# Kernel optimization log

Hardware: AMD Instinct MI355X
Metric: run time of the kernel (lower is better)

The kernel has to match this reference:

```python
import jax, jax.numpy as jnp
from jax import lax
import numpy as np

B, T, I, H, O = 64, 1024, 256, 512, 128


def setup_inputs() -> dict:
    key = jax.random.key(0)
    ks = jax.random.split(key, 12)
    s_i = 1.0 / np.sqrt(H)
    return {
        "x": jax.random.normal(ks[0], (B, T, I), dtype=jnp.float32),
        "h0": jnp.zeros((2, B, H), dtype=jnp.float32),
        # layer 0 RNNCell(I -> H)
        "W_ih0": jax.random.uniform(ks[1], (H, I), jnp.float32, -s_i, s_i),
        "b_ih0": jax.random.uniform(ks[2], (H,), jnp.float32, -s_i, s_i),
        "W_hh0": jax.random.uniform(ks[3], (H, H), jnp.float32, -s_i, s_i),
        "b_hh0": jax.random.uniform(ks[4], (H,), jnp.float32, -s_i, s_i),
        # layer 1 RNNCell(H -> H)
        "W_ih1": jax.random.uniform(ks[5], (H, H), jnp.float32, -s_i, s_i),
        "b_ih1": jax.random.uniform(ks[6], (H,), jnp.float32, -s_i, s_i),
        "W_hh1": jax.random.uniform(ks[7], (H, H), jnp.float32, -s_i, s_i),
        "b_hh1": jax.random.uniform(ks[8], (H,), jnp.float32, -s_i, s_i),
        # final Linear(H -> O) applied to last timestep hidden
        "W_out": jax.random.uniform(ks[9], (O, H), jnp.float32, -s_i, s_i),
        "b_out": jax.random.uniform(ks[10], (O,), jnp.float32, -s_i, s_i),
    }


def reference(x, h0, W_ih0, b_ih0, W_hh0, b_hh0, W_ih1, b_ih1, W_hh1, b_hh1, W_out, b_out):
    # x: [B, T, I]; h0: [2, B, H]. Stacked tanh RNN cells over time, then
    # Linear head on the last timestep's top-layer hidden (outs[-1]).
    def step(carry, x_t):
        h_0, h_1 = carry  # each [B, H]
        h_0 = jnp.tanh(x_t @ W_ih0.T + b_ih0 + h_0 @ W_hh0.T + b_hh0)
        h_1 = jnp.tanh(h_0 @ W_ih1.T + b_ih1 + h_1 @ W_hh1.T + b_hh1)
        return (h_0, h_1), None

    x_tbi = jnp.swapaxes(x, 0, 1)  # [T, B, I] for scan over time
    (h_0, h_1), _ = lax.scan(step, (h0[0], h0[1]), x_tbi)
    out = h_1 @ W_out.T + b_out  # [B, O]
    return out
```

## Files before the change

### kernel.cpp

```cpp
#include <hip/hip_runtime.h>
#include <hip/hip_bf16.h>

#define TT 1024
#define BB 64
#define II 256
#define HH 512
#define OO 128

typedef __attribute__((ext_vector_type(4))) float f32x4;
typedef __attribute__((ext_vector_type(4))) int   i32x4;
typedef __attribute__((ext_vector_type(8))) __bf16 bf16x8;
typedef __attribute__((ext_vector_type(8))) short s16x8;
typedef unsigned long long u64;
typedef unsigned short u16;
typedef unsigned int u32;

#define BIAS_OFF 132096
#define SMEM_BYTES 132608

static __device__ __forceinline__ u16 f2b(float f) { return __builtin_bit_cast(u16, (__bf16)f); }
static __device__ __forceinline__ float b2f(u16 u) { return (float)__builtin_bit_cast(__bf16, u); }

static __device__ __forceinline__ u64 pack4f(float a, float b, float c, float d) {
    return (u64)f2b(a) | ((u64)f2b(b) << 16) | ((u64)f2b(c) << 32) | ((u64)f2b(d) << 48);
}
static __device__ __forceinline__ bf16x8 cvt8(f32x4 a0, f32x4 a1) {
    bf16x8 v;
    v[0]=(__bf16)a0[0]; v[1]=(__bf16)a0[1]; v[2]=(__bf16)a0[2]; v[3]=(__bf16)a0[3];
    v[4]=(__bf16)a1[0]; v[5]=(__bf16)a1[1]; v[6]=(__bf16)a1[2]; v[7]=(__bf16)a1[3];
    return v;
}
static __device__ __forceinline__ void spin_ge(int* c, int tgt) {
    while (__hip_atomic_load(c, __ATOMIC_RELAXED, __HIP_MEMORY_SCOPE_AGENT) < tgt)
        __builtin_amdgcn_s_sleep(1);
}
static __device__ __forceinline__ u64 ald(const u64* p) {
    return __hip_atomic_load(p, __ATOMIC_RELAXED, __HIP_MEMORY_SCOPE_AGENT);
}
static __device__ __forceinline__ void ast(u64* p, u64 v) {
    __hip_atomic_store(p, v, __ATOMIC_RELAXED, __HIP_MEMORY_SCOPE_AGENT);
}

__global__ __launch_bounds__(512, 2) void xproj_kernel(
    const float* __restrict__ x, const float* __restrict__ Wih0,
    const float* __restrict__ bih0, const float* __restrict__ bhh0,
    u64* __restrict__ XBu)
{
    const int tid = threadIdx.x;
    const int l = tid & 63, w = tid >> 6;
    const int lm = l & 15, lg = l >> 4;
    const int t = blockIdx.x * 4 + (w >> 1);
    const int nh = w & 1;

    bf16x8 xf[4][8];
    #pragma unroll
    for (int bt = 0; bt < 4; ++bt) {
        const float* xb = x + (size_t)(bt * 16 + lm) * (TT * II) + (size_t)t * II + lg * 8;
        #pragma unroll
        for (int kt = 0; kt < 8; ++kt) {
            f32x4 a0 = *(const f32x4*)(xb + kt * 32);
            f32x4 a1 = *(const f32x4*)(xb + kt * 32 + 4);
            xf[bt][kt] = cvt8(a0, a1);
        }
    }
    for (int nt = 0; nt < 16; ++nt) {
        const int n_row = nh * 256 + nt * 16 + lm;
        bf16x8 wf[8];
        #pragma unroll
        for (int kt = 0; kt < 8; ++kt) {
            const float* wsrc = Wih0 + (size_t)n_row * II + kt * 32 + lg * 8;
            f32x4 a0 = *(const f32x4*)(wsrc);
            f32x4 a1 = *(const f32x4*)(wsrc + 4);
            wf[kt] = cvt8(a0, a1);
        }
        f32x4 acc[4] = {{0,0,0,0},{0,0,0,0},{0,0,0,0},{0,0,0,0}};
        #pragma unroll
        for (int kt = 0; kt < 8; ++kt)
            #pragma unroll
            for (int bt = 0; bt < 4; ++bt)
                acc[bt] = __builtin_amdgcn_mfma_f32_16x16x32_bf16(wf[kt], xf[bt][kt], acc[bt], 0, 0, 0);
        const int n0 = nh * 256 + nt * 16 + lg * 4;
        f32x4 bias = *(const f32x4*)(bih0 + n0);
        f32x4 bias2 = *(const f32x4*)(bhh0 + n0);
        #pragma unroll
        for (int bt = 0; bt < 4; ++bt) {
            const int b = bt * 16 + lm;
            XBu[((size_t)t * 64 + b) * 128 + (n0 >> 2)] =
                pack4f(acc[bt][0] + bias[0] + bias2[0], acc[bt][1] + bias[1] + bias2[1],
                       acc[bt][2] + bias[2] + bias2[2], acc[bt][3] + bias[3] + bias2[3]);
        }
    }
}

template <int L>
static __device__ void run_layer(const u16* __restrict__ XB,
                                 const float* __restrict__ hinit,
                                 const float* __restrict__ Wi,
                                 const float* __restrict__ Wh,
                                 const float* __restrict__ bi, const float* __restrict__ bh,
                                 int* cnt0, int* cnt1,
                                 u64* h0s, u64* h1s,
                                 int nb, char* smem)
{
    constexpr int KT = (L == 0) ? 16 : 32;
    constexpr int NGRP = (L == 0) ? 1 : 2;
    constexpr int MTW = (L == 0) ? 1 : 2;
    constexpr int WKG = (L == 0) ? 2 : 4;
    constexpr int PART_OFF = (L == 0) ? 65536 : 0;

    const int tid = threadIdx.x;
    const int l = tid & 63, w = tid >> 6;
    const int lm = l & 15, lg = l >> 4;
    const int wm = (L == 0) ? (w & 3) : (w & 1);
    const int wk = (L == 0) ? (w >> 2) : (w >> 1);
    u64* wbase = (L == 0) ? h0s : h1s;
    int* mycnt = (L == 0) ? cnt0 : cnt1;

    {
        const int m = tid >> 3, c0 = (tid & 7) * 8;
        const float* s = hinit + (size_t)m * HH + nb + c0;
        u64* d = &wbase[3 * 8192 + m * 128 + (nb >> 2) + (tid & 7) * 2];
        ast(&d[0], pack4f(s[0], s[1], s[2], s[3]));
        ast(&d[1], pack4f(s[4], s[5], s[6], s[7]));
    }
    if (L == 1 && tid < 64) {
        float* bias_l = (float*)(smem + BIAS_OFF);
        bias_l[tid] = bi[nb + tid] + bh[nb + tid];
    }
    __syncthreads();
    if (tid == 0) {
        __builtin_amdgcn_fence(__ATOMIC_RELEASE, "agent");
        __hip_atomic_fetch_add(mycnt, 1, __ATOMIC_RELAXED, __HIP_MEMORY_SCOPE_AGENT);
    }

    bf16x8 B[4][8];
    #pragma unroll
    for (int nt = 0; nt < 4; ++nt) {
        const int n = nb + nt * 16 + lm;
        #pragma unroll
        for (int ktl = 0; ktl < 8; ++ktl) {
            const int ktg = wk * 8 + ktl;
            const float* src;
            if (L == 0) src = Wi + (size_t)n * HH + ktg * 32 + lg * 8;
            else        src = (ktg < 16) ? (Wi + (size_t)n * HH + ktg * 32 + lg * 8)
                                         : (Wh + (size_t)n * HH + (ktg - 16) * 32 + lg * 8);
            f32x4 a0 = *(const f32x4*)(src);
            f32x4 a1 = *(const f32x4*)(src + 4);
            B[nt][ktl] = cvt8(a0, a1);
        }
    }

    for (int t = 0; t < TT; ++t) {
        if (tid == 0) {
            if (L == 0) {
                spin_ge(cnt0, 8 * (t + 1));
                if (t >= 4) spin_ge(cnt1, 8 * (t - 2));
            } else {
                spin_ge(cnt0, 8 * (t + 2));
                spin_ge(cnt1, 8 * (t + 1));
            }
        }
        __syncthreads();
        __builtin_amdgcn_fence(__ATOMIC_ACQUIRE, "agent");

        const u64* src0 = h0s + ((L == 0 ? (t + 3) : t) & 3) * 8192;
        const u64* src1 = h1s + ((t + 3) & 3) * 8192;
        #pragma unroll
        for (int g = 0; g < NGRP; ++g) {
            const u64* sp = (g == 0) ? src0 : src1;
            i32x4 tmp[8];
            #pragma unroll
            for (int p = 0; p < 8; ++p) {
                const int s = p * 512 + tid;
                const int m = s & 63, c = s >> 6;
                tmp[p] = *(const i32x4*)(sp + m * 128 + c * 2);
            }
            #pragma unroll
            for (int p = 0; p < 8; ++p) {
                const int s = p * 512 + tid;
                const int m = s & 63, c = s >> 6;
                const int fa = (m >> 4) * KT + g * 16 + (c >> 2);
                const int ll = ((c & 3) << 4) | (m & 15);
                *(i32x4*)(smem + fa * 1024 + ll * 16) = tmp[p];
            }
        }
        __syncthreads();

        f32x4 acc[MTW][4];
        #pragma unroll
        for (int i = 0; i < MTW; ++i)
            #pragma unroll
            for (int nt = 0; nt < 4; ++nt) acc[i][nt] = f32x4{0, 0, 0, 0};
        #pragma unroll
        for (int ktl = 0; ktl < 8; ++ktl) {
            #pragma unroll
            for (int i = 0; i < MTW; ++i) {
                const int fa = (wm * MTW + i) * KT + wk * 8 + ktl;
                bf16x8 a = *(const bf16x8*)(smem + fa * 1024 + l * 16);
                #pragma unroll
                for (int nt = 0; nt < 4; ++nt)
                    acc[i][nt] = __builtin_amdgcn_mfma_f32_16x16x32_bf16(a, B[nt][ktl], acc[i][nt], 0, 0, 0);
            }
        }
        if (L == 1) __syncthreads();

        float* part = (float*)(smem + PART_OFF);
        #pragma unroll
        for (int i = 0; i < MTW; ++i)
            #pragma unroll
            for (int nt = 0; nt < 4; ++nt)
                #pragma unroll
                for (int r = 0; r < 4; ++r) {
                    const int m = (wm * MTW + i) * 16 + lg * 4 + r;
                    part[(wk * 64 + m) * 64 + nt * 16 + lm] = acc[i][nt][r];
                }
        __syncthreads();

        {
            const int m = tid >> 3, c0 = (tid & 7) * 8;
            f32x4 sa = {0, 0, 0, 0}, sb = {0, 0, 0, 0};
            #pragma unroll
            for (int k = 0; k < WKG; ++k) {
                const float* pr = part + (k * 64 + m) * 64 + c0;
                sa += *(const f32x4*)pr;
                sb += *(const f32x4*)(pr + 4);
            }
            float e[8];
            if (L == 0) {
                const s16x8 xv = *(const s16x8*)(XB + ((size_t)t * 64 + m) * 512 + nb + c0);
                #pragma unroll
                for (int r = 0; r < 4; ++r) {
                    e[r] = sa[r] + b2f((u16)xv[r]);
                    e[4 + r] = sb[r] + b2f((u16)xv[4 + r]);
                }
            } else {
                const float* bl = (const float*)(smem + BIAS_OFF) + c0;
                #pragma unroll
                for (int r = 0; r < 4; ++r) {
                    e[r] = sa[r] + bl[r];
                    e[4 + r] = sb[r] + bl[4 + r];
                }
            }
            u64* d = &wbase[(t & 3) * 8192 + m * 128 + (nb >> 2) + (tid & 7) * 2];
            ast(&d[0], pack4f(tanhf(e[0]), tanhf(e[1]), tanhf(e[2]), tanhf(e[3])));
            ast(&d[1], pack4f(tanhf(e[4]), tanhf(e[5]), tanhf(e[6]), tanhf(e[7])));
        }
        __syncthreads();
        if (tid == 0) {
            __builtin_amdgcn_fence(__ATOMIC_RELEASE, "agent");
            __hip_atomic_fetch_add(mycnt, 1, __ATOMIC_RELAXED, __HIP_MEMORY_SCOPE_AGENT);
        }
    }
}

static __device__ void head_phase(const float* __restrict__ Wout,
                                  const float* __restrict__ bout,
                                  const u64* __restrict__ h1slot,
                                  float* __restrict__ out,
                                  int obase, int* cnt1, char* smem)
{
    const int tid = threadIdx.x;
    if (tid == 0) spin_ge(cnt1, 8 * (TT + 1));
    __syncthreads();
    __builtin_amdgcn_fence(__ATOMIC_ACQUIRE, "agent");
    float* hf = (float*)smem;
    for (int q = tid; q < 8192; q += 512) {
        u64 v = ald(&h1slot[q]);
        const int m = q >> 7, c4 = (q & 127) * 4;
        float* d = hf + m * 516 + c4;
        d[0] = b2f((u16)v);         d[1] = b2f((u16)(v >> 16));
        d[2] = b2f((u16)(v >> 32)); d[3] = b2f((u16)(v >> 48));
    }
    __syncthreads();
    const int b = tid >> 3, oo = tid & 7;
    const float* hrow = hf + b * 516;
    #pragma unroll
    for (int h = 0; h < 2; ++h) {
        const int o = obase + oo + h * 8;
        const float* wr = Wout + (size_t)o * HH;
        float acc = 0.f;
        #pragma unroll 4
        for (int k4 = 0; k4 < 128; ++k4) {
            f32x4 wv = *(const f32x4*)(wr + k4 * 4);
            f32x4 hv = *(const f32x4*)(hrow + k4 * 4);
            acc += wv[0]*hv[0] + wv[1]*hv[1] + wv[2]*hv[2] + wv[3]*hv[3];
        }
        out[b * OO + o] = acc + bout[o];
    }
}

__global__ __launch_bounds__(512, 2) void rnn_persist(
    const u16* __restrict__ XB,
    const float* __restrict__ h0init,
    const float* __restrict__ Whh0,
    const float* __restrict__ Wih1, const float* __restrict__ bih1,
    const float* __restrict__ Whh1, const float* __restrict__ bhh1,
    const float* __restrict__ Wout, const float* __restrict__ bout,
    float* __restrict__ out, int* __restrict__ cnt, u64* __restrict__ hbuf)
{
    __shared__ __align__(16) char smem[SMEM_BYTES];
    const int bx = blockIdx.x;
    int* cnt0 = cnt;
    int* cnt1 = cnt + 32;
    u64* h0s = hbuf;
    u64* h1s = hbuf + 4 * 8192;
    if (bx < 8) {
        run_layer<0>(XB, h0init, Whh0, nullptr, nullptr, nullptr,
                     cnt0, cnt1, h0s, h1s, bx * 64, smem);
    } else {
        run_layer<1>(nullptr, h0init + BB * HH, Wih1, Whh1, bih1, bhh1,
                     cnt0, cnt1, h0s, h1s, (bx - 8) * 64, smem);
        head_phase(Wout, bout, h1s + 3 * 8192, out, (bx - 8) * 16, cnt1, smem);
    }
}

extern "C" void kernel_launch(void* const* d_in, const int* in_sizes, int n_in,
                              void* d_out, int out_size, void* d_ws, size_t ws_size,
                              hipStream_t stream) {
    const float* x     = (const float*)d_in[0];
    const float* h0i   = (const float*)d_in[1];
    const float* Wih0  = (const float*)d_in[2];
    const float* bih0  = (const float*)d_in[3];
    const float* Whh0  = (const float*)d_in[4];
    const float* bhh0  = (const float*)d_in[5];
    const float* Wih1  = (const float*)d_in[6];
    const float* bih1  = (const float*)d_in[7];
    const float* Whh1  = (const float*)d_in[8];
    const float* bhh1  = (const float*)d_in[9];
    const float* Wout  = (const float*)d_in[10];
    const float* bout  = (const float*)d_in[11];
    float* out = (float*)d_out;

    int* cnt  = (int*)d_ws;
    u64* hbuf = (u64*)((char*)d_ws + 256);
    u16* XB   = (u16*)((char*)d_ws + (1 << 20));

    hipMemsetAsync(d_ws, 0, 256, stream);
    xproj_kernel<<<256, 512, 0, stream>>>(x, Wih0, bih0, bhh0, (u64*)XB);

    void* args[] = { &XB, &h0i, &Whh0, &Wih1, &bih1, &Whh1, &bhh1,
                     &Wout, &bout, &out, &cnt, &hbuf };
    hipLaunchCooperativeKernel((const void*)rnn_persist, dim3(16), dim3(512),
                               args, 0, stream);
}
```

Before: 8.964 ms.

## Load recurrent state straight from global into MFMA operands, per-wave spin waits

```diff
diff --git a/kernel.cpp b/kernel.cpp
--- a/kernel.cpp
+++ b/kernel.cpp
@@ -9,6 +9,7 @@
 
 typedef __attribute__((ext_vector_type(4))) float f32x4;
 typedef __attribute__((ext_vector_type(4))) int   i32x4;
+typedef __attribute__((ext_vector_type(2))) unsigned long long u64x2;
 typedef __attribute__((ext_vector_type(8))) __bf16 bf16x8;
 typedef __attribute__((ext_vector_type(8))) short s16x8;
 typedef unsigned long long u64;
@@ -30,9 +31,12 @@
     v[4]=(__bf16)a1[0]; v[5]=(__bf16)a1[1]; v[6]=(__bf16)a1[2]; v[7]=(__bf16)a1[3];
     return v;
 }
-static __device__ __forceinline__ void spin_ge(int* c, int tgt) {
-    while (__hip_atomic_load(c, __ATOMIC_RELAXED, __HIP_MEMORY_SCOPE_AGENT) < tgt)
-        __builtin_amdgcn_s_sleep(1);
+static __device__ __forceinline__ bf16x8 mk8(u64 lo, u64 hi) {
+    u64x2 v; v[0] = lo; v[1] = hi;
+    return __builtin_bit_cast(bf16x8, v);
+}
+static __device__ __forceinline__ int ald32(const int* p) {
+    return __hip_atomic_load(p, __ATOMIC_RELAXED, __HIP_MEMORY_SCOPE_AGENT);
 }
 static __device__ __forceinline__ u64 ald(const u64* p) {
     return __hip_atomic_load(p, __ATOMIC_RELAXED, __HIP_MEMORY_SCOPE_AGENT);
@@ -102,11 +106,8 @@
                                  u64* h0s, u64* h1s,
                                  int nb, char* smem)
 {
-    constexpr int KT = (L == 0) ? 16 : 32;
-    constexpr int NGRP = (L == 0) ? 1 : 2;
+    constexpr int WKG = (L == 0) ? 2 : 4;
     constexpr int MTW = (L == 0) ? 1 : 2;
-    constexpr int WKG = (L == 0) ? 2 : 4;
-    constexpr int PART_OFF = (L == 0) ? 65536 : 0;
 
     const int tid = threadIdx.x;
     const int l = tid & 63, w = tid >> 6;
@@ -117,21 +118,18 @@
     int* mycnt = (L == 0) ? cnt0 : cnt1;
 
     {
-        const int m = tid >> 3, c0 = (tid & 7) * 8;
-        const float* s = hinit + (size_t)m * HH + nb + c0;
-        u64* d = &wbase[3 * 8192 + m * 128 + (nb >> 2) + (tid & 7) * 2];
+        const int m = tid >> 3, c8 = tid & 7;
+        const float* s = hinit + (size_t)m * HH + nb + c8 * 8;
+        u64* d = &wbase[3 * 8192 + m * 128 + (nb >> 2) + c8 * 2];
         ast(&d[0], pack4f(s[0], s[1], s[2], s[3]));
         ast(&d[1], pack4f(s[4], s[5], s[6], s[7]));
     }
-    if (L == 1 && tid < 64) {
-        float* bias_l = (float*)(smem + BIAS_OFF);
-        bias_l[tid] = bi[nb + tid] + bh[nb + tid];
-    }
+    if (L == 1 && tid < 64)
+        ((float*)(smem + BIAS_OFF))[tid] = bi[nb + tid] + bh[nb + tid];
+    asm volatile("s_waitcnt vmcnt(0)" ::: "memory");
     __syncthreads();
-    if (tid == 0) {
-        __builtin_amdgcn_fence(__ATOMIC_RELEASE, "agent");
+    if (tid == 0)
         __hip_atomic_fetch_add(mycnt, 1, __ATOMIC_RELAXED, __HIP_MEMORY_SCOPE_AGENT);
-    }
 
     bf16x8 B[4][8];
     #pragma unroll
@@ -150,61 +148,83 @@
         }
     }
 
+    float* part = (float*)smem;
+
     for (int t = 0; t < TT; ++t) {
-        if (tid == 0) {
-            if (L == 0) {
-                spin_ge(cnt0, 8 * (t + 1));
-                if (t >= 4) spin_ge(cnt1, 8 * (t - 2));
+        f32x4 acc[MTW][4];
+        #pragma unroll
+        for (int i = 0; i < MTW; ++i)
+            #pragma unroll
+            for (int nt = 0; nt < 4; ++nt) acc[i][nt] = f32x4{0, 0, 0, 0};
+
+        if (L == 0) {
+            const int tgt = 8 * (t + 1);
+            while (ald32(cnt0) < tgt) {}
+            if (t >= 4) { const int tg1 = 8 * (t - 2); while (ald32(cnt1) < tg1) {} }
+            asm volatile("" ::: "memory");
+            const u64* sp = h0s + ((t + 3) & 3) * 8192
+                          + (wm * 16 + lm) * 128 + wk * 64 + lg * 2;
+            u64 pa[8][2];
+            #pragma unroll
+            for (int ktl = 0; ktl < 8; ++ktl) {
+                pa[ktl][0] = ald(sp + ktl * 8);
+                pa[ktl][1] = ald(sp + ktl * 8 + 1);
+            }
+            #pragma unroll
+            for (int ktl = 0; ktl < 8; ++ktl) {
+                bf16x8 a = mk8(pa[ktl][0], pa[ktl][1]);
+                #pragma unroll
+                for (int nt = 0; nt < 4; ++nt)
+                    acc[0][nt] = __builtin_amdgcn_mfma_f32_16x16x32_bf16(a, B[nt][ktl], acc[0][nt], 0, 0, 0);
+            }
+        } else {
+            if (wk >= 2) {
+                const int tgt = 8 * (t + 1);
+                while (ald32(cnt1) < tgt) {}
+                asm volatile("" ::: "memory");
+                const u64* sp = h1s + ((t + 3) & 3) * 8192 + (wk - 2) * 64 + lg * 2;
+                #pragma unroll
+                for (int i = 0; i < MTW; ++i) {
+                    const u64* spm = sp + ((wm * 2 + i) * 16 + lm) * 128;
+                    u64 pa[8][2];
+                    #pragma unroll
+                    for (int ktl = 0; ktl < 8; ++ktl) {
+                        pa[ktl][0] = ald(spm + ktl * 8);
+                        pa[ktl][1] = ald(spm + ktl * 8 + 1);
+                    }
+                    #pragma unroll
+                    for (int ktl = 0; ktl < 8; ++ktl) {
+                        bf16x8 a = mk8(pa[ktl][0], pa[ktl][1]);
+                        #pragma unroll
+                        for (int nt = 0; nt < 4; ++nt)
+                            acc[i][nt] = __builtin_amdgcn_mfma_f32_16x16x32_bf16(a, B[nt][ktl], acc[i][nt], 0, 0, 0);
+                    }
+                }
             } else {
-                spin_ge(cnt0, 8 * (t + 2));
-                spin_ge(cnt1, 8 * (t + 1));
-            }
-        }
-        __syncthreads();
-        __builtin_amdgcn_fence(__ATOMIC_ACQUIRE, "agent");
-
-        const u64* src0 = h0s + ((L == 0 ? (t + 3) : t) & 3) * 8192;
-        const u64* src1 = h1s + ((t + 3) & 3) * 8192;
-        #pragma unroll
-        for (int g = 0; g < NGRP; ++g) {
-            const u64* sp = (g == 0) ? src0 : src1;
-            i32x4 tmp[8];
-            #pragma unroll
-            for (int p = 0; p < 8; ++p) {
-                const int s = p * 512 + tid;
-                const int m = s & 63, c = s >> 6;
-                tmp[p] = *(const i32x4*)(sp + m * 128 + c * 2);
-            }
-            #pragma unroll
-            for (int p = 0; p < 8; ++p) {
-                const int s = p * 512 + tid;
-                const int m = s & 63, c = s >> 6;
-                const int fa = (m >> 4) * KT + g * 16 + (c >> 2);
-                const int ll = ((c & 3) << 4) | (m & 15);
-                *(i32x4*)(smem + fa * 1024 + ll * 16) = tmp[p];
-            }
-        }
-        __syncthreads();
-
-        f32x4 acc[MTW][4];
-        #pragma unroll
-        for (int i = 0; i < MTW; ++i)
-            #pragma unroll
-            for (int nt = 0; nt < 4; ++nt) acc[i][nt] = f32x4{0, 0, 0, 0};
-        #pragma unroll
-        for (int ktl = 0; ktl < 8; ++ktl) {
-            #pragma unroll
-            for (int i = 0; i < MTW; ++i) {
-                const int fa = (wm * MTW + i) * KT + wk * 8 + ktl;
-                bf16x8 a = *(const bf16x8*)(smem + fa * 1024 + l * 16);
-                #pragma unroll
-                for (int nt = 0; nt < 4; ++nt)
-                    acc[i][nt] = __builtin_amdgcn_mfma_f32_16x16x32_bf16(a, B[nt][ktl], acc[i][nt], 0, 0, 0);
-            }
-        }
-        if (L == 1) __syncthreads();
-
-        float* part = (float*)(smem + PART_OFF);
+                const int tgt = 8 * (t + 2);
+                while (ald32(cnt0) < tgt) {}
+                asm volatile("" ::: "memory");
+                const u64* sp = h0s + (t & 3) * 8192 + wk * 64 + lg * 2;
+                #pragma unroll
+                for (int i = 0; i < MTW; ++i) {
+                    const u64* spm = sp + ((wm * 2 + i) * 16 + lm) * 128;
+                    u64 pa[8][2];
+                    #pragma unroll
+                    for (int ktl = 0; ktl < 8; ++ktl) {
+                        pa[ktl][0] = ald(spm + ktl * 8);
+                        pa[ktl][1] = ald(spm + ktl * 8 + 1);
+                    }
+                    #pragma unroll
+                    for (int ktl = 0; ktl < 8; ++ktl) {
+                        bf16x8 a = mk8(pa[ktl][0], pa[ktl][1]);
+                        #pragma unroll
+                        for (int nt = 0; nt < 4; ++nt)
+                            acc[i][nt] = __builtin_amdgcn_mfma_f32_16x16x32_bf16(a, B[nt][ktl], acc[i][nt], 0, 0, 0);
+                    }
+                }
+            }
+        }
+
         #pragma unroll
         for (int i = 0; i < MTW; ++i)
             #pragma unroll
@@ -245,11 +265,10 @@
             ast(&d[0], pack4f(tanhf(e[0]), tanhf(e[1]), tanhf(e[2]), tanhf(e[3])));
             ast(&d[1], pack4f(tanhf(e[4]), tanhf(e[5]), tanhf(e[6]), tanhf(e[7])));
         }
+        asm volatile("s_waitcnt vmcnt(0)" ::: "memory");
         __syncthreads();
-        if (tid == 0) {
-            __builtin_amdgcn_fence(__ATOMIC_RELEASE, "agent");
+        if (tid == 0)
             __hip_atomic_fetch_add(mycnt, 1, __ATOMIC_RELAXED, __HIP_MEMORY_SCOPE_AGENT);
-        }
     }
 }
 
@@ -260,9 +279,9 @@
                                   int obase, int* cnt1, char* smem)
 {
     const int tid = threadIdx.x;
-    if (tid == 0) spin_ge(cnt1, 8 * (TT + 1));
+    if (tid == 0) { while (ald32(cnt1) < 8 * (TT + 1)) {} }
     __syncthreads();
-    __builtin_amdgcn_fence(__ATOMIC_ACQUIRE, "agent");
+    asm volatile("" ::: "memory");
     float* hf = (float*)smem;
     for (int q = tid; q < 8192; q += 512) {
         u64 v = ald(&h1slot[q]);
```

Result: slower. 9.572 ms (+6.8%).
